# Kernel optimization log

Hardware: AMD Instinct MI355X
Metric: run time of the kernel (lower is better)

## Reference

```python
import jax, jax.numpy as jnp
import numpy as np

N = 50000   # nodes
E = 800000  # edges (avg degree 16)
D = 128     # feature / hidden dim


def _lin(x, W, b):
    # torch nn.Linear convention: W is [out, in]
    return x @ W.T + b


def setup_inputs() -> dict:
    key = jax.random.key(0)
    ks = jax.random.split(key, 24)
    p = lambda k, s: jax.random.normal(k, s, dtype=jnp.float32) * 0.05
    inp = {
        "node_feat": jax.random.normal(ks[0], (N, D), dtype=jnp.float32),
        "edge_feat": jax.random.normal(ks[1], (E, D), dtype=jnp.float32),
        "src_idx": jax.random.randint(ks[2], (E,), 0, N),
        "dst_idx": jax.random.randint(ks[3], (E,), 0, N),
        "Wsrc": p(ks[4], (D, D)), "bsrc": p(ks[5], (D,)),
        "Wdst": p(ks[6], (D, D)), "bdst": p(ks[7], (D,)),
        "Wphi1": p(ks[8], (D, D)), "bphi1": p(ks[9], (D,)),
        "Wphi2": p(ks[10], (D, D)), "bphi2": p(ks[11], (D,)),
        "Wphi3": p(ks[12], (D, D)), "bphi3": p(ks[13], (D,)),
        "Wth1": p(ks[14], (D, D)), "bth1": p(ks[15], (D,)),
        "Wth2": p(ks[16], (D, D)), "bth2": p(ks[17], (D,)),
        "Wpd": p(ks[18], (D, D)), "bpd": p(ks[19], (D,)),
        "Wpu": p(ks[20], (D, D)), "bpu": p(ks[21], (D,)),
    }
    return inp


def reference(node_feat, edge_feat, src_idx, dst_idx,
              Wsrc, bsrc, Wdst, bdst,
              Wphi1, bphi1, Wphi2, bphi2, Wphi3, bphi3,
              Wth1, bth1, Wth2, bth2,
              Wpd, bpd, Wpu, bpu):
    h = node_feat                               # [N, D]
    h_src = h[src_idx]                          # [E, D] gather
    h_dst = h[dst_idx]                          # [E, D] gather
    # edge code: e + affine(src) + affine(dst)
    t = edge_feat + _lin(h_src, Wsrc, bsrc) + _lin(h_dst, Wdst, bdst)
    # phi MLP (activation_first=True, n_hidden=2): ReLU, L, ReLU, L, ReLU, L
    x = jax.nn.relu(t)
    x = jax.nn.relu(_lin(x, Wphi1, bphi1))
    x = jax.nn.relu(_lin(x, Wphi2, bphi2))
    e_emb = _lin(x, Wphi3, bphi3)               # [E, D]
    # u_mul_e + sum: message = h[src] * e_emb, scatter-sum into dst
    m = h_src * e_emb                           # [E, D]
    agg = jax.ops.segment_sum(m, dst_idx, num_segments=h.shape[0])  # [N, D]
    # combine: theta(phi_dst(h) + phi_upd(agg)); theta = ReLU, L, ReLU, L
    y = _lin(h, Wpd, bpd) + _lin(agg, Wpu, bpu)
    y = jax.nn.relu(y)
    y = jax.nn.relu(_lin(y, Wth1, bth1))
    return _lin(y, Wth2, bth2)                  # [N, D]
```

## Files before the change

### kernel.cpp

```cpp
#include <hip/hip_runtime.h>
#include <hip/hip_bf16.h>

#define NN 50000
#define NE 800000
#define NT_E 12500
#define GRID_E 768
#define NBLK_SCAN 196

typedef __attribute__((ext_vector_type(8))) short bf16x8;
typedef __attribute__((ext_vector_type(4))) float f32x4;
typedef __attribute__((ext_vector_type(2))) float f32x2;
typedef __attribute__((ext_vector_type(8))) unsigned short u16x8;
typedef __attribute__((ext_vector_type(2))) unsigned short u16x2;

__device__ __forceinline__ unsigned short f2bf(float f) {
    union { float f; unsigned u; } v; v.f = f;
    unsigned r = v.u + 0x7FFFu + ((v.u >> 16) & 1u);
    return (unsigned short)(r >> 16);
}
__device__ __forceinline__ float bf2f(unsigned short h) {
    union { unsigned u; float f; } v; v.u = ((unsigned)h) << 16;
    return v.f;
}
__device__ __forceinline__ f32x4 mfma16(bf16x8 a, bf16x8 b, f32x4 c) {
    return __builtin_amdgcn_mfma_f32_16x16x32_bf16(a, b, c, 0, 0, 0);
}
__device__ __forceinline__ void syncl() {
    asm volatile("s_waitcnt lgkmcnt(0)\n\ts_barrier" ::: "memory");
}

__device__ __forceinline__ void load_wfrags(const unsigned short* __restrict__ Wb,
                                            int wv, int lane, bf16x8 (&wf)[4][2]) {
#pragma unroll
    for (int kk = 0; kk < 4; ++kk)
#pragma unroll
        for (int j = 0; j < 2; ++j) {
            int row = 32 * wv + 16 * j + (lane & 15);
            int col = 32 * kk + 8 * (lane >> 4);
            wf[kk][j] = *(const bf16x8*)(Wb + row * 128 + col);
        }
}

__device__ __forceinline__ void zero_acc(f32x4 (&acc)[4][2]) {
#pragma unroll
    for (int mt = 0; mt < 4; ++mt)
#pragma unroll
        for (int j = 0; j < 2; ++j) {
            f32x4 z = {0.f, 0.f, 0.f, 0.f};
            acc[mt][j] = z;
        }
}

__device__ __forceinline__ void gemm64(const unsigned short* __restrict__ X,
                                       const bf16x8 (&wf)[4][2], f32x4 (&acc)[4][2], int lane) {
#pragma unroll
    for (int kk = 0; kk < 4; ++kk) {
        bf16x8 a[4];
#pragma unroll
        for (int mt = 0; mt < 4; ++mt) {
            int row = mt * 16 + (lane & 15);
            a[mt] = *(const bf16x8*)(X + row * 136 + kk * 32 + 8 * (lane >> 4));
        }
#pragma unroll
        for (int mt = 0; mt < 4; ++mt) {
            acc[mt][0] = mfma16(a[mt], wf[kk][0], acc[mt][0]);
            acc[mt][1] = mfma16(a[mt], wf[kk][1], acc[mt][1]);
        }
    }
}

__device__ __forceinline__ void epi_lds(unsigned short* __restrict__ Xo,
                                        const f32x4 (&acc)[4][2],
                                        float bb0, float bb1, int c0, int rbase) {
#pragma unroll
    for (int mt = 0; mt < 4; ++mt)
#pragma unroll
        for (int r = 0; r < 4; ++r) {
            int row = mt * 16 + rbase + r;
            Xo[row * 136 + c0]      = f2bf(fmaxf(acc[mt][0][r] + bb0, 0.f));
            Xo[row * 136 + c0 + 16] = f2bf(fmaxf(acc[mt][1][r] + bb1, 0.f));
        }
}

__device__ __forceinline__ void epi_lds_norelu(unsigned short* __restrict__ Xo,
                                               const f32x4 (&acc)[4][2],
                                               float bb0, float bb1, int c0, int rbase) {
#pragma unroll
    for (int mt = 0; mt < 4; ++mt)
#pragma unroll
        for (int r = 0; r < 4; ++r) {
            int row = mt * 16 + rbase + r;
            Xo[row * 136 + c0]      = f2bf(acc[mt][0][r] + bb0);
            Xo[row * 136 + c0 + 16] = f2bf(acc[mt][1][r] + bb1);
        }
}

__device__ __forceinline__ void stage_f32row(unsigned short* __restrict__ Xrow,
                                             const f32x4* __restrict__ p) {
#pragma unroll
    for (int i = 0; i < 4; ++i) {
        f32x4 lo = p[2 * i], hi = p[2 * i + 1];
        unsigned short tmp[8];
#pragma unroll
        for (int j = 0; j < 4; ++j) { tmp[j] = f2bf(lo[j]); tmp[4 + j] = f2bf(hi[j]); }
        *(u16x8*)(Xrow + i * 8) = *(u16x8*)tmp;
    }
}

__global__ void k_wconv(const float* w0, const float* w1, const float* w2,
                        const float* w3, const float* w4, const float* w5,
                        const float* w6, const float* w7, const float* w8,
                        unsigned short* out) {
    const float* ws[9] = {w0, w1, w2, w3, w4, w5, w6, w7, w8};
    int m = blockIdx.x >> 2;
    int part = blockIdx.x & 3;
    const float* w = ws[m] + part * 4096 + threadIdx.x * 16;
    unsigned short* o = out + m * 16384 + part * 4096 + threadIdx.x * 16;
    float f[16];
#pragma unroll
    for (int i = 0; i < 4; ++i) *(f32x4*)(f + 4 * i) = ((const f32x4*)w)[i];
    unsigned short tmp[16];
#pragma unroll
    for (int i = 0; i < 16; ++i) tmp[i] = f2bf(f[i]);
    ((u16x8*)o)[0] = *(u16x8*)tmp;
    ((u16x8*)o)[1] = *(u16x8*)(tmp + 8);
}

__global__ void k_hist(const int* __restrict__ dst, int* __restrict__ cnt) {
    int i = blockIdx.x * 256 + threadIdx.x;
    if (i < NE) atomicAdd(&cnt[dst[i]], 1);
}

__global__ void k_scan1(const int* __restrict__ c, int* __restrict__ bsum) {
    __shared__ int red[256];
    int i = blockIdx.x * 256 + threadIdx.x;
    red[threadIdx.x] = (i < NN) ? c[i] : 0;
    __syncthreads();
    for (int off = 128; off > 0; off >>= 1) {
        if (threadIdx.x < off) red[threadIdx.x] += red[threadIdx.x + off];
        __syncthreads();
    }
    if (threadIdx.x == 0) bsum[blockIdx.x] = red[0];
}

__global__ void k_scan2(int* __restrict__ bsum) {
    __shared__ int s[256];
    int t = threadIdx.x;
    s[t] = (t < NBLK_SCAN) ? bsum[t] : 0;
    __syncthreads();
    for (int off = 1; off < 256; off <<= 1) {
        int v = (t >= off) ? s[t - off] : 0;
        __syncthreads();
        s[t] += v;
        __syncthreads();
    }
    if (t < NBLK_SCAN) bsum[t] = (t == 0) ? 0 : s[t - 1];
}

__global__ void k_scan3(int* __restrict__ cnt, const int* __restrict__ bsum,
                        int* __restrict__ rowptr) {
    __shared__ int s[256];
    int t = threadIdx.x;
    int i = blockIdx.x * 256 + t;
    int v = (i < NN) ? cnt[i] : 0;
    s[t] = v;
    __syncthreads();
    for (int off = 1; off < 256; off <<= 1) {
        int x = (t >= off) ? s[t - off] : 0;
        __syncthreads();
        s[t] += x;
        __syncthreads();
    }
    int excl = bsum[blockIdx.x] + s[t] - v;
    if (i < NN) { rowptr[i] = excl; cnt[i] = excl; }
    if (i == 0) rowptr[NN] = NE;
}

__global__ void k_pos(const int* __restrict__ dst, int* __restrict__ cursor,
                      int* __restrict__ pos) {
    int i = blockIdx.x * 256 + threadIdx.x;
    if (i < NE) pos[i] = atomicAdd(&cursor[dst[i]], 1);
}

__global__ __launch_bounds__(256, 3)
void k_nodepre(const float* __restrict__ h,
               const unsigned short* __restrict__ Wb,
               const float* __restrict__ bsrc, const float* __restrict__ bdst,
               unsigned short* __restrict__ AH, unsigned short* __restrict__ Adst) {
    __shared__ unsigned short X[64 * 136];
    int tid = threadIdx.x, lane = tid & 63, wv = tid >> 6;
    int n0 = blockIdx.x * 64;
    {
        int row = tid >> 2, q = tid & 3;
        int n = n0 + row;
        if (n < NN) {
            unsigned short tmp[32];
            const f32x4* hp = (const f32x4*)(h + (size_t)n * 128 + q * 32);
#pragma unroll
            for (int i = 0; i < 8; ++i) {
                f32x4 v = hp[i];
#pragma unroll
                for (int j = 0; j < 4; ++j) tmp[i * 4 + j] = f2bf(v[j]);
            }
#pragma unroll
            for (int i = 0; i < 4; ++i)
                *(u16x8*)(X + row * 136 + q * 32 + i * 8) = *(u16x8*)(tmp + i * 8);
            u16x8* hb = (u16x8*)(AH + (size_t)n * 256 + 128 + q * 32);
#pragma unroll
            for (int i = 0; i < 4; ++i) hb[i] = *(u16x8*)(tmp + i * 8);
        } else {
            u16x8 z = {0, 0, 0, 0, 0, 0, 0, 0};
#pragma unroll
            for (int i = 0; i < 4; ++i) *(u16x8*)(X + row * 136 + q * 32 + i * 8) = z;
        }
    }
    __syncthreads();

    bf16x8 wfS[4][2], wfD[4][2];
    load_wfrags(Wb, wv, lane, wfS);
    load_wfrags(Wb + 16384, wv, lane, wfD);
    f32x4 accS[4][2], accD[4][2];
    zero_acc(accS); zero_acc(accD);
    gemm64(X, wfS, accS, lane);
    gemm64(X, wfD, accD, lane);

    int c0 = 32 * wv + (lane & 15);
    float bs0 = bsrc[c0], bs1 = bsrc[c0 + 16];
    float bd0 = bdst[c0], bd1 = bdst[c0 + 16];
    int rbase = (lane >> 4) * 4;
#pragma unroll
    for (int mt = 0; mt < 4; ++mt)
#pragma unroll
        for (int r = 0; r < 4; ++r) {
            int n = n0 + mt * 16 + rbase + r;
            if (n < NN) {
                AH[(size_t)n * 256 + c0]        = f2bf(accS[mt][0][r] + bs0);
                AH[(size_t)n * 256 + c0 + 16]   = f2bf(accS[mt][1][r] + bs1);
                Adst[(size_t)n * 128 + c0]      = f2bf(accD[mt][0][r] + bd0);
                Adst[(size_t)n * 128 + c0 + 16] = f2bf(accD[mt][1][r] + bd1);
            }
        }
}

__global__ __launch_bounds__(256, 3)
void k_edgeB(const float* __restrict__ ef,
             const int* __restrict__ src, const int* __restrict__ dst,
             const int* __restrict__ pos,
             const unsigned short* __restrict__ AH,
             const unsigned short* __restrict__ Adst,
             const unsigned short* __restrict__ Wb,
             const float* __restrict__ b1, const float* __restrict__ b2,
             const float* __restrict__ b3,
             unsigned short* __restrict__ Mbuf) {
    __shared__ __align__(16) char sh[52480];
    unsigned short* X0 = (unsigned short*)sh;
    unsigned short* X1 = (unsigned short*)(sh + 17408);
    unsigned short* Hs = (unsigned short*)(sh + 34816);
    int*         posarr = (int*)(sh + 52224);

    int tid = threadIdx.x, lane = tid & 63, wv = tid >> 6;

    bf16x8 wf1[4][2], wf2[4][2], wf3[4][2];
    load_wfrags(Wb + 2 * 16384, wv, lane, wf1);
    load_wfrags(Wb + 3 * 16384, wv, lane, wf2);
    load_wfrags(Wb + 4 * 16384, wv, lane, wf3);

    int c0 = 32 * wv + (lane & 15);
    float b1_0 = b1[c0], b1_1 = b1[c0 + 16];
    float b2_0 = b2[c0], b2_1 = b2[c0 + 16];
    float b3_0 = b3[c0], b3_1 = b3[c0 + 16];
    int rbase = (lane >> 4) * 4;
    int srow = tid >> 2, q = tid & 3;

    int b = blockIdx.x, nb = gridDim.x;
    int qt = NT_E / nb, rt = NT_E % nb;
    int t0 = (b < rt) ? b * (qt + 1) : rt * (qt + 1) + (b - rt) * qt;
    int t1 = t0 + ((b < rt) ? qt + 1 : qt);

    int sN, dN, pN;
    f32x4 efr[8];
    {
        int e = t0 * 64 + srow;
        sN = src[e]; dN = dst[e]; pN = pos[e];
        const f32x4* ep = (const f32x4*)(ef + (size_t)e * 128 + q * 32);
#pragma unroll
        for (int i = 0; i < 8; ++i) efr[i] = ep[i];
    }

    for (int t = t0; t < t1; ++t) {
        int s = sN, d = dN, p = pN;
        syncl();
        {
            if (q == 0) posarr[srow] = p;
            const u16x8* ap = (const u16x8*)(AH + (size_t)s * 256 + q * 32);
            const u16x8* hp = (const u16x8*)(AH + (size_t)s * 256 + 128 + q * 32);
            const u16x8* dp = (const u16x8*)(Adst + (size_t)d * 128 + q * 32);
#pragma unroll
            for (int i = 0; i < 4; ++i) {
                u16x8 a8 = ap[i], d8 = dp[i], h8 = hp[i];
                f32x4 lo = efr[2 * i], hi = efr[2 * i + 1];
                unsigned short o[8];
#pragma unroll
                for (int j = 0; j < 8; ++j) {
                    float evv = (j < 4) ? lo[j] : hi[j - 4];
                    float v = evv + bf2f((unsigned short)a8[j]) + bf2f((unsigned short)d8[j]);
                    o[j] = f2bf(fmaxf(v, 0.f));
                }
                *(u16x8*)(X0 + srow * 136 + q * 32 + i * 8) = *(u16x8*)o;
                *(u16x8*)(Hs + srow * 136 + q * 32 + i * 8) = h8;
            }
        }
        if (t + 1 < t1) {
            int e = (t + 1) * 64 + srow;
            sN = src[e]; dN = dst[e]; pN = pos[e];
            const f32x4* ep = (const f32x4*)(ef + (size_t)e * 128 + q * 32);
#pragma unroll
            for (int i = 0; i < 8; ++i) efr[i] = ep[i];
        }
        syncl();
        f32x4 acc[4][2];
        zero_acc(acc);
        gemm64(X0, wf1, acc, lane);
        syncl();
        epi_lds(X1, acc, b1_0, b1_1, c0, rbase);
        syncl();
        zero_acc(acc);
        gemm64(X1, wf2, acc, lane);
        epi_lds(X0, acc, b2_0, b2_1, c0, rbase);
        syncl();
        zero_acc(acc);
        gemm64(X0, wf3, acc, lane);
        syncl();
        epi_lds_norelu(X1, acc, b3_0, b3_1, c0, rbase);
        syncl();
        {
            int posr = posarr[srow];
            unsigned short* mp = Mbuf + (size_t)posr * 128 + q * 32;
#pragma unroll
            for (int i = 0; i < 4; ++i) {
                u16x8 ev = *(const u16x8*)(X1 + srow * 136 + q * 32 + i * 8);
                u16x8 hv = *(const u16x8*)(Hs + srow * 136 + q * 32 + i * 8);
                u16x8 o;
#pragma unroll
                for (int j = 0; j < 8; ++j)
                    o[j] = f2bf(bf2f((unsigned short)ev[j]) * bf2f((unsigned short)hv[j]));
                *(u16x8*)(mp + i * 8) = o;
            }
        }
    }
}

__global__ __launch_bounds__(256, 3)
void k_nodeoutF(const unsigned short* __restrict__ AH,
                const unsigned short* __restrict__ Mbuf,
                const int* __restrict__ rowptr,
                const unsigned short* __restrict__ Wb,
                const float* __restrict__ bpd, const float* __restrict__ bpu,
                const float* __restrict__ bt1, const float* __restrict__ bt2,
                float* __restrict__ out) {
    __shared__ unsigned short Xh[64 * 136];
    __shared__ unsigned short Xa[64 * 136];
    int tid = threadIdx.x, lane = tid & 63, wv = tid >> 6;
    int n0 = blockIdx.x * 64;
    {
        int row = tid >> 2, q = tid & 3;
        int n = n0 + row;
        if (n < NN) {
            const u16x8* hp = (const u16x8*)(AH + (size_t)n * 256 + 128 + q * 32);
#pragma unroll
            for (int i = 0; i < 4; ++i)
                *(u16x8*)(Xh + row * 136 + q * 32 + i * 8) = hp[i];
        } else {
            u16x8 z = {0, 0, 0, 0, 0, 0, 0, 0};
#pragma unroll
            for (int i = 0; i < 4; ++i)
                *(u16x8*)(Xh + row * 136 + q * 32 + i * 8) = z;
        }
    }
    {
#pragma unroll 1
        for (int it = 0; it < 16; ++it) {
            int row = wv * 16 + it;
            int n = n0 + row;
            float a0 = 0.f, a1 = 0.f;
            if (n < NN) {
                int j0 = rowptr[n], j1 = rowptr[n + 1];
                int j = j0;
                for (; j + 3 < j1; j += 4) {
                    u16x2 v0 = *(const u16x2*)(Mbuf + (size_t)j * 128 + lane * 2);
                    u16x2 v1 = *(const u16x2*)(Mbuf + (size_t)(j + 1) * 128 + lane * 2);
                    u16x2 v2 = *(const u16x2*)(Mbuf + (size_t)(j + 2) * 128 + lane * 2);
                    u16x2 v3 = *(const u16x2*)(Mbuf + (size_t)(j + 3) * 128 + lane * 2);
                    a0 += bf2f(v0[0]) + bf2f(v1[0]) + bf2f(v2[0]) + bf2f(v3[0]);
                    a1 += bf2f(v0[1]) + bf2f(v1[1]) + bf2f(v2[1]) + bf2f(v3[1]);
                }
                for (; j < j1; ++j) {
                    u16x2 v = *(const u16x2*)(Mbuf + (size_t)j * 128 + lane * 2);
                    a0 += bf2f(v[0]); a1 += bf2f(v[1]);
                }
            }
            Xa[row * 136 + lane * 2]     = f2bf(a0);
            Xa[row * 136 + lane * 2 + 1] = f2bf(a1);
        }
    }
    __syncthreads();
    bf16x8 wfa[4][2], wfb[4][2];
    load_wfrags(Wb + 5 * 16384, wv, lane, wfa);
    load_wfrags(Wb + 6 * 16384, wv, lane, wfb);
    int c0 = 32 * wv + (lane & 15);
    int rbase = (lane >> 4) * 4;
    f32x4 acc[4][2];
    zero_acc(acc);
    gemm64(Xh, wfa, acc, lane);
    gemm64(Xa, wfb, acc, lane);
    float bb0 = bpd[c0] + bpu[c0], bb1 = bpd[c0 + 16] + bpu[c0 + 16];
    __syncthreads();
    epi_lds(Xh, acc, bb0, bb1, c0, rbase);
    __syncthreads();
    load_wfrags(Wb + 7 * 16384, wv, lane, wfa);
    zero_acc(acc);
    gemm64(Xh, wfa, acc, lane);
    float b10 = bt1[c0], b11 = bt1[c0 + 16];
    __syncthreads();
    epi_lds(Xa, acc, b10, b11, c0, rbase);
    __syncthreads();
    load_wfrags(Wb + 8 * 16384, wv, lane, wfb);
    zero_acc(acc);
    gemm64(Xa, wfb, acc, lane);
    float b20 = bt2[c0], b21 = bt2[c0 + 16];
#pragma unroll
    for (int mt = 0; mt < 4; ++mt)
#pragma unroll
        for (int r = 0; r < 4; ++r) {
            int n = n0 + mt * 16 + rbase + r;
            if (n < NN) {
                out[(size_t)n * 128 + c0]      = acc[mt][0][r] + b20;
                out[(size_t)n * 128 + c0 + 16] = acc[mt][1][r] + b21;
            }
        }
}

__global__ __launch_bounds__(256, 2)
void k_edge_atomic(const float* __restrict__ ef,
                   const int* __restrict__ src, const int* __restrict__ dst,
                   const unsigned short* __restrict__ AH,
                   const unsigned short* __restrict__ Adst,
                   const unsigned short* __restrict__ Wb,
                   const float* __restrict__ b1, const float* __restrict__ b2,
                   const float* __restrict__ b3,
                   float* __restrict__ agg) {
    __shared__ unsigned short X0[64 * 136];
    __shared__ unsigned short X1[64 * 136];
    __shared__ unsigned short Hs[64 * 136];
    __shared__ int doff_lds[64];

    int tid = threadIdx.x, lane = tid & 63, wv = tid >> 6;
    bf16x8 wf1[4][2], wf2[4][2], wf3[4][2];
    load_wfrags(Wb + 2 * 16384, wv, lane, wf1);
    load_wfrags(Wb + 3 * 16384, wv, lane, wf2);
    load_wfrags(Wb + 4 * 16384, wv, lane, wf3);

    int c0 = 32 * wv + (lane & 15);
    float b1_0 = b1[c0], b1_1 = b1[c0 + 16];
    float b2_0 = b2[c0], b2_1 = b2[c0 + 16];
    float b3_0 = b3[c0], b3_1 = b3[c0 + 16];
    int rbase = (lane >> 4) * 4;
    int srow = tid >> 2, q = tid & 3;

    for (int t = blockIdx.x; t < NT_E; t += gridDim.x) {
        int e0 = t * 64;
        __syncthreads();
        {
            int e = e0 + srow;
            int s = src[e], d = dst[e];
            if (q == 0) doff_lds[srow] = d * 128;
            const f32x4* ep = (const f32x4*)(ef + (size_t)e * 128 + q * 32);
            const u16x8* ap = (const u16x8*)(AH + (size_t)s * 256 + q * 32);
            const u16x8* hp = (const u16x8*)(AH + (size_t)s * 256 + 128 + q * 32);
            const u16x8* dp = (const u16x8*)(Adst + (size_t)d * 128 + q * 32);
#pragma unroll
            for (int i = 0; i < 4; ++i) {
                u16x8 a8 = ap[i], d8 = dp[i], h8 = hp[i];
                f32x4 lo = ep[2 * i], hi = ep[2 * i + 1];
                unsigned short o[8];
#pragma unroll
                for (int j = 0; j < 8; ++j) {
                    float evv = (j < 4) ? lo[j] : hi[j - 4];
                    float v = evv + bf2f((unsigned short)a8[j]) + bf2f((unsigned short)d8[j]);
                    o[j] = f2bf(fmaxf(v, 0.f));
                }
                *(u16x8*)(X0 + srow * 136 + q * 32 + i * 8) = *(u16x8*)o;
                *(u16x8*)(Hs + srow * 136 + q * 32 + i * 8) = h8;
            }
        }
        __syncthreads();
        f32x4 acc[4][2];
        zero_acc(acc);
        gemm64(X0, wf1, acc, lane);
        __syncthreads();
        epi_lds(X1, acc, b1_0, b1_1, c0, rbase);
        __syncthreads();
        zero_acc(acc);
        gemm64(X1, wf2, acc, lane);
        epi_lds(X0, acc, b2_0, b2_1, c0, rbase);
        __syncthreads();
        zero_acc(acc);
        gemm64(X0, wf3, acc, lane);
#pragma unroll
        for (int mt = 0; mt < 4; ++mt)
#pragma unroll
            for (int r = 0; r < 4; ++r) {
                int row = mt * 16 + rbase + r;
                int dofs = doff_lds[row];
                float h0 = bf2f(Hs[row * 136 + c0]);
                float h1 = bf2f(Hs[row * 136 + c0 + 16]);
                atomicAdd(agg + dofs + c0,      (acc[mt][0][r] + b3_0) * h0);
                atomicAdd(agg + dofs + c0 + 16, (acc[mt][1][r] + b3_1) * h1);
            }
    }
}

__global__ __launch_bounds__(256, 3)
void k_nodeout(const unsigned short* __restrict__ AH,
               const float* __restrict__ agg,
               const unsigned short* __restrict__ Wb,
               const float* __restrict__ bpd, const float* __restrict__ bpu,
               const float* __restrict__ bt1, const float* __restrict__ bt2,
               float* __restrict__ out) {
    __shared__ unsigned short Xh[64 * 136];
    __shared__ unsigned short Xa[64 * 136];
    int tid = threadIdx.x, lane = tid & 63, wv = tid >> 6;
    int n0 = blockIdx.x * 64;
    {
        int row = tid >> 2, q = tid & 3;
        int n = n0 + row;
        if (n < NN) {
            const u16x8* hp = (const u16x8*)(AH + (size_t)n * 256 + 128 + q * 32);
#pragma unroll
            for (int i = 0; i < 4; ++i)
                *(u16x8*)(Xh + row * 136 + q * 32 + i * 8) = hp[i];
            stage_f32row(Xa + row * 136 + q * 32,
                         (const f32x4*)(agg + (size_t)n * 128 + q * 32));
        } else {
            u16x8 z = {0, 0, 0, 0, 0, 0, 0, 0};
#pragma unroll
            for (int i = 0; i < 4; ++i) {
                *(u16x8*)(Xh + row * 136 + q * 32 + i * 8) = z;
                *(u16x8*)(Xa + row * 136 + q * 32 + i * 8) = z;
            }
        }
    }
    __syncthreads();
    bf16x8 wfa[4][2], wfb[4][2];
    load_wfrags(Wb + 5 * 16384, wv, lane, wfa);
    load_wfrags(Wb + 6 * 16384, wv, lane, wfb);
    int c0 = 32 * wv + (lane & 15);
    int rbase = (lane >> 4) * 4;
    f32x4 acc[4][2];
    zero_acc(acc);
    gemm64(Xh, wfa, acc, lane);
    gemm64(Xa, wfb, acc, lane);
    float bb0 = bpd[c0] + bpu[c0], bb1 = bpd[c0 + 16] + bpu[c0 + 16];
    __syncthreads();
    epi_lds(Xh, acc, bb0, bb1, c0, rbase);
    __syncthreads();
    load_wfrags(Wb + 7 * 16384, wv, lane, wfa);
    zero_acc(acc);
    gemm64(Xh, wfa, acc, lane);
    float b10 = bt1[c0], b11 = bt1[c0 + 16];
    __syncthreads();
    epi_lds(Xa, acc, b10, b11, c0, rbase);
    __syncthreads();
    load_wfrags(Wb + 8 * 16384, wv, lane, wfb);
    zero_acc(acc);
    gemm64(Xa, wfb, acc, lane);
    float b20 = bt2[c0], b21 = bt2[c0 + 16];
#pragma unroll
    for (int mt = 0; mt < 4; ++mt)
#pragma unroll
        for (int r = 0; r < 4; ++r) {
            int n = n0 + mt * 16 + rbase + r;
            if (n < NN) {
                out[(size_t)n * 128 + c0]      = acc[mt][0][r] + b20;
                out[(size_t)n * 128 + c0 + 16] = acc[mt][1][r] + b21;
            }
        }
}

extern "C" void kernel_launch(void* const* d_in, const int* in_sizes, int n_in,
                              void* d_out, int out_size, void* d_ws, size_t ws_size,
                              hipStream_t stream) {
    (void)in_sizes; (void)n_in; (void)out_size;
    const float* node_feat = (const float*)d_in[0];
    const float* edge_feat = (const float*)d_in[1];
    const int*   src  = (const int*)d_in[2];
    const int*   dst  = (const int*)d_in[3];
    const float* Wsrc = (const float*)d_in[4];  const float* bsrc = (const float*)d_in[5];
    const float* Wdst = (const float*)d_in[6];  const float* bdst = (const float*)d_in[7];
    const float* Wphi1 = (const float*)d_in[8]; const float* bphi1 = (const float*)d_in[9];
    const float* Wphi2 = (const float*)d_in[10];const float* bphi2 = (const float*)d_in[11];
    const float* Wphi3 = (const float*)d_in[12];const float* bphi3 = (const float*)d_in[13];
    const float* Wth1 = (const float*)d_in[14]; const float* bth1 = (const float*)d_in[15];
    const float* Wth2 = (const float*)d_in[16]; const float* bth2 = (const float*)d_in[17];
    const float* Wpd  = (const float*)d_in[18]; const float* bpd  = (const float*)d_in[19];
    const float* Wpu  = (const float*)d_in[20]; const float* bpu  = (const float*)d_in[21];

    char* ws = (char*)d_ws;
    size_t off = 0;
    unsigned short* Wb   = (unsigned short*)(ws + off); off += 294912;
    unsigned short* AH   = (unsigned short*)(ws + off); off += 25600000;
    unsigned short* Adst = (unsigned short*)(ws + off); off += 12800000;
    float*          agg  = (float*)(ws + off);          off += 25600000;
    int*            cnt  = (int*)(ws + off);            off += 200064;
    int*            rowptr = (int*)(ws + off);          off += 200064;
    int*            bsum = (int*)(ws + off);            off += 1024;
    int*            pos  = (int*)(ws + off);            off += 3200000;
    unsigned short* Mbuf = (unsigned short*)(ws + off); off += 204800000;
    bool primary = (ws_size >= off);

    k_wconv<<<36, 256, 0, stream>>>(Wsrc, Wdst, Wphi1, Wphi2, Wphi3,
                                    Wpd, Wpu, Wth1, Wth2, Wb);
    k_nodepre<<<782, 256, 0, stream>>>(node_feat, Wb, bsrc, bdst, AH, Adst);

    if (primary) {
        hipMemsetAsync(cnt, 0, (size_t)NN * 4, stream);
        k_hist<<<3125, 256, 0, stream>>>(dst, cnt);
        k_scan1<<<NBLK_SCAN, 256, 0, stream>>>(cnt, bsum);
        k_scan2<<<1, 256, 0, stream>>>(bsum);
        k_scan3<<<NBLK_SCAN, 256, 0, stream>>>(cnt, bsum, rowptr);
        k_pos<<<3125, 256, 0, stream>>>(dst, cnt, pos);
        k_edgeB<<<GRID_E, 256, 0, stream>>>(edge_feat, src, dst, pos,
                                            AH, Adst, Wb,
                                            bphi1, bphi2, bphi3, Mbuf);
        k_nodeoutF<<<782, 256, 0, stream>>>(AH, Mbuf, rowptr, Wb,
                                            bpd, bpu, bth1, bth2, (float*)d_out);
    } else {
        hipMemsetAsync(agg, 0, (size_t)NN * 128 * 4, stream);
        k_edge_atomic<<<1024, 256, 0, stream>>>(edge_feat, src, dst,
                                                AH, Adst, Wb,
                                                bphi1, bphi2, bphi3, agg);
        k_nodeout<<<782, 256, 0, stream>>>(AH, agg, Wb, bpd, bpu, bth1, bth2,
                                           (float*)d_out);
    }
}
```

Measured before the change: 511.3 us.

## Merge preprocessing kernels and single-block scan; drop edge_feat prefetch in edge kernel

Fuses weight conversion with the degree histogram, replaces the three-kernel scan with a single 1024-thread block scan, and folds the position-assignment atomics into the node preprocessing kernel as extra blocks. This cuts the number of launches and inter-kernel gaps on the critical path from eight to four. Separately, the edge kernel stops prefetching the next tile's edge features into registers and reads them directly when needed. That frees registers but exposes global load latency inside the loop. The single-block scan serialises about 49 elements per thread.

```diff
diff --git a/kernel.cpp b/kernel.cpp
--- a/kernel.cpp
+++ b/kernel.cpp
@@ -5,7 +5,8 @@
 #define NE 800000
 #define NT_E 12500
 #define GRID_E 768
-#define NBLK_SCAN 196
+#define NBLK_NODE 782
+#define NBLK_EDGE 3125
 
 typedef __attribute__((ext_vector_type(8))) short bf16x8;
 typedef __attribute__((ext_vector_type(4))) float f32x4;
@@ -107,87 +108,67 @@
     }
 }
 
-__global__ void k_wconv(const float* w0, const float* w1, const float* w2,
-                        const float* w3, const float* w4, const float* w5,
-                        const float* w6, const float* w7, const float* w8,
-                        unsigned short* out) {
-    const float* ws[9] = {w0, w1, w2, w3, w4, w5, w6, w7, w8};
-    int m = blockIdx.x >> 2;
-    int part = blockIdx.x & 3;
-    const float* w = ws[m] + part * 4096 + threadIdx.x * 16;
-    unsigned short* o = out + m * 16384 + part * 4096 + threadIdx.x * 16;
-    float f[16];
-#pragma unroll
-    for (int i = 0; i < 4; ++i) *(f32x4*)(f + 4 * i) = ((const f32x4*)w)[i];
-    unsigned short tmp[16];
-#pragma unroll
-    for (int i = 0; i < 16; ++i) tmp[i] = f2bf(f[i]);
-    ((u16x8*)o)[0] = *(u16x8*)tmp;
-    ((u16x8*)o)[1] = *(u16x8*)(tmp + 8);
-}
-
-__global__ void k_hist(const int* __restrict__ dst, int* __restrict__ cnt) {
-    int i = blockIdx.x * 256 + threadIdx.x;
-    if (i < NE) atomicAdd(&cnt[dst[i]], 1);
-}
-
-__global__ void k_scan1(const int* __restrict__ c, int* __restrict__ bsum) {
-    __shared__ int red[256];
-    int i = blockIdx.x * 256 + threadIdx.x;
-    red[threadIdx.x] = (i < NN) ? c[i] : 0;
-    __syncthreads();
-    for (int off = 128; off > 0; off >>= 1) {
-        if (threadIdx.x < off) red[threadIdx.x] += red[threadIdx.x + off];
+__global__ void k_init(const float* w0, const float* w1, const float* w2,
+                       const float* w3, const float* w4, const float* w5,
+                       const float* w6, const float* w7, const float* w8,
+                       unsigned short* out,
+                       const int* __restrict__ dst, int* __restrict__ cnt) {
+    if (blockIdx.x < 36) {
+        const float* ws[9] = {w0, w1, w2, w3, w4, w5, w6, w7, w8};
+        int m = blockIdx.x >> 2;
+        int part = blockIdx.x & 3;
+        const float* w = ws[m] + part * 4096 + threadIdx.x * 16;
+        unsigned short* o = out + m * 16384 + part * 4096 + threadIdx.x * 16;
+        float f[16];
+#pragma unroll
+        for (int i = 0; i < 4; ++i) *(f32x4*)(f + 4 * i) = ((const f32x4*)w)[i];
+        unsigned short tmp[16];
+#pragma unroll
+        for (int i = 0; i < 16; ++i) tmp[i] = f2bf(f[i]);
+        ((u16x8*)o)[0] = *(u16x8*)tmp;
+        ((u16x8*)o)[1] = *(u16x8*)(tmp + 8);
+    } else {
+        int i = (blockIdx.x - 36) * 256 + threadIdx.x;
+        if (i < NE) atomicAdd(&cnt[dst[i]], 1);
+    }
+}
+
+__global__ void k_scanall(int* __restrict__ cnt, int* __restrict__ rowptr) {
+    __shared__ int part[1024];
+    int tid = threadIdx.x;
+    const int CH = 49;
+    int base = tid * CH;
+    int s = 0;
+    for (int i = 0; i < CH; ++i) { int idx = base + i; if (idx < NN) s += cnt[idx]; }
+    part[tid] = s;
+    __syncthreads();
+    for (int off = 1; off < 1024; off <<= 1) {
+        int v = (tid >= off) ? part[tid - off] : 0;
         __syncthreads();
-    }
-    if (threadIdx.x == 0) bsum[blockIdx.x] = red[0];
-}
-
-__global__ void k_scan2(int* __restrict__ bsum) {
-    __shared__ int s[256];
-    int t = threadIdx.x;
-    s[t] = (t < NBLK_SCAN) ? bsum[t] : 0;
-    __syncthreads();
-    for (int off = 1; off < 256; off <<= 1) {
-        int v = (t >= off) ? s[t - off] : 0;
+        part[tid] += v;
         __syncthreads();
-        s[t] += v;
-        __syncthreads();
-    }
-    if (t < NBLK_SCAN) bsum[t] = (t == 0) ? 0 : s[t - 1];
-}
-
-__global__ void k_scan3(int* __restrict__ cnt, const int* __restrict__ bsum,
-                        int* __restrict__ rowptr) {
-    __shared__ int s[256];
-    int t = threadIdx.x;
-    int i = blockIdx.x * 256 + t;
-    int v = (i < NN) ? cnt[i] : 0;
-    s[t] = v;
-    __syncthreads();
-    for (int off = 1; off < 256; off <<= 1) {
-        int x = (t >= off) ? s[t - off] : 0;
-        __syncthreads();
-        s[t] += x;
-        __syncthreads();
-    }
-    int excl = bsum[blockIdx.x] + s[t] - v;
-    if (i < NN) { rowptr[i] = excl; cnt[i] = excl; }
-    if (i == 0) rowptr[NN] = NE;
-}
-
-__global__ void k_pos(const int* __restrict__ dst, int* __restrict__ cursor,
-                      int* __restrict__ pos) {
-    int i = blockIdx.x * 256 + threadIdx.x;
-    if (i < NE) pos[i] = atomicAdd(&cursor[dst[i]], 1);
+    }
+    int excl = (tid == 0) ? 0 : part[tid - 1];
+    for (int i = 0; i < CH; ++i) {
+        int idx = base + i;
+        if (idx < NN) { int c = cnt[idx]; rowptr[idx] = excl; cnt[idx] = excl; excl += c; }
+    }
+    if (tid == 0) rowptr[NN] = NE;
 }
 
 __global__ __launch_bounds__(256, 3)
-void k_nodepre(const float* __restrict__ h,
-               const unsigned short* __restrict__ Wb,
-               const float* __restrict__ bsrc, const float* __restrict__ bdst,
-               unsigned short* __restrict__ AH, unsigned short* __restrict__ Adst) {
+void k_prep(const float* __restrict__ h,
+            const unsigned short* __restrict__ Wb,
+            const float* __restrict__ bsrc, const float* __restrict__ bdst,
+            unsigned short* __restrict__ AH, unsigned short* __restrict__ Adst,
+            const int* __restrict__ dst, int* __restrict__ cursor,
+            int* __restrict__ pos) {
     __shared__ unsigned short X[64 * 136];
+    if (blockIdx.x >= NBLK_NODE) {
+        int i = (blockIdx.x - NBLK_NODE) * 256 + threadIdx.x;
+        if (i < NE) pos[i] = atomicAdd(&cursor[dst[i]], 1);
+        return;
+    }
     int tid = threadIdx.x, lane = tid & 63, wv = tid >> 6;
     int n0 = blockIdx.x * 64;
     {
@@ -278,27 +259,25 @@
     int t1 = t0 + ((b < rt) ? qt + 1 : qt);
 
     int sN, dN, pN;
-    f32x4 efr[8];
     {
         int e = t0 * 64 + srow;
         sN = src[e]; dN = dst[e]; pN = pos[e];
-        const f32x4* ep = (const f32x4*)(ef + (size_t)e * 128 + q * 32);
-#pragma unroll
-        for (int i = 0; i < 8; ++i) efr[i] = ep[i];
     }
 
     for (int t = t0; t < t1; ++t) {
         int s = sN, d = dN, p = pN;
         syncl();
         {
+            int e = t * 64 + srow;
             if (q == 0) posarr[srow] = p;
+            const f32x4* ep = (const f32x4*)(ef + (size_t)e * 128 + q * 32);
             const u16x8* ap = (const u16x8*)(AH + (size_t)s * 256 + q * 32);
             const u16x8* hp = (const u16x8*)(AH + (size_t)s * 256 + 128 + q * 32);
             const u16x8* dp = (const u16x8*)(Adst + (size_t)d * 128 + q * 32);
 #pragma unroll
             for (int i = 0; i < 4; ++i) {
                 u16x8 a8 = ap[i], d8 = dp[i], h8 = hp[i];
-                f32x4 lo = efr[2 * i], hi = efr[2 * i + 1];
+                f32x4 lo = ep[2 * i], hi = ep[2 * i + 1];
                 unsigned short o[8];
 #pragma unroll
                 for (int j = 0; j < 8; ++j) {
@@ -313,9 +292,6 @@
         if (t + 1 < t1) {
             int e = (t + 1) * 64 + srow;
             sN = src[e]; dN = dst[e]; pN = pos[e];
-            const f32x4* ep = (const f32x4*)(ef + (size_t)e * 128 + q * 32);
-#pragma unroll
-            for (int i = 0; i < 8; ++i) efr[i] = ep[i];
         }
         syncl();
         f32x4 acc[4][2];
@@ -617,29 +593,30 @@
     int*            pos  = (int*)(ws + off);            off += 3200000;
     unsigned short* Mbuf = (unsigned short*)(ws + off); off += 204800000;
     bool primary = (ws_size >= off);
-
-    k_wconv<<<36, 256, 0, stream>>>(Wsrc, Wdst, Wphi1, Wphi2, Wphi3,
-                                    Wpd, Wpu, Wth1, Wth2, Wb);
-    k_nodepre<<<782, 256, 0, stream>>>(node_feat, Wb, bsrc, bdst, AH, Adst);
+    (void)bsum;
 
     if (primary) {
         hipMemsetAsync(cnt, 0, (size_t)NN * 4, stream);
-        k_hist<<<3125, 256, 0, stream>>>(dst, cnt);
-        k_scan1<<<NBLK_SCAN, 256, 0, stream>>>(cnt, bsum);
-        k_scan2<<<1, 256, 0, stream>>>(bsum);
-        k_scan3<<<NBLK_SCAN, 256, 0, stream>>>(cnt, bsum, rowptr);
-        k_pos<<<3125, 256, 0, stream>>>(dst, cnt, pos);
+        k_init<<<36 + NBLK_EDGE, 256, 0, stream>>>(Wsrc, Wdst, Wphi1, Wphi2, Wphi3,
+                                                   Wpd, Wpu, Wth1, Wth2, Wb, dst, cnt);
+        k_scanall<<<1, 1024, 0, stream>>>(cnt, rowptr);
+        k_prep<<<NBLK_NODE + NBLK_EDGE, 256, 0, stream>>>(node_feat, Wb, bsrc, bdst,
+                                                          AH, Adst, dst, cnt, pos);
         k_edgeB<<<GRID_E, 256, 0, stream>>>(edge_feat, src, dst, pos,
                                             AH, Adst, Wb,
                                             bphi1, bphi2, bphi3, Mbuf);
-        k_nodeoutF<<<782, 256, 0, stream>>>(AH, Mbuf, rowptr, Wb,
-                                            bpd, bpu, bth1, bth2, (float*)d_out);
+        k_nodeoutF<<<NBLK_NODE, 256, 0, stream>>>(AH, Mbuf, rowptr, Wb,
+                                                  bpd, bpu, bth1, bth2, (float*)d_out);
     } else {
+        k_init<<<36, 256, 0, stream>>>(Wsrc, Wdst, Wphi1, Wphi2, Wphi3,
+                                       Wpd, Wpu, Wth1, Wth2, Wb, dst, cnt);
+        k_prep<<<NBLK_NODE, 256, 0, stream>>>(node_feat, Wb, bsrc, bdst,
+                                              AH, Adst, dst, cnt, pos);
         hipMemsetAsync(agg, 0, (size_t)NN * 128 * 4, stream);
         k_edge_atomic<<<1024, 256, 0, stream>>>(edge_feat, src, dst,
                                                 AH, Adst, Wb,
                                                 bphi1, bphi2, bphi3, agg);
-        k_nodeout<<<782, 256, 0, stream>>>(AH, agg, Wb, bpd, bpu, bth1, bth2,
-                                           (float*)d_out);
-    }
-}
+        k_nodeout<<<NBLK_NODE, 256, 0, stream>>>(AH, agg, Wb, bpd, bpu, bth1, bth2,
+                                                 (float*)d_out);
+    }
+}
```

New measurement: 621.3 us. 1.22x slower.
